# Optimization experiments

Hardware: AMD Instinct MI355X
Metric: run time of the kernel (lower is better)

The kernel has to match this reference:

```python
import jax, jax.numpy as jnp
import numpy as np

N_NODES = 100000
N_EDGES = 6400000


def setup_inputs() -> dict:
    key = jax.random.key(0)
    ks = jax.random.split(key, 20)
    g = lambda i, shape, fan_in: jax.random.normal(ks[i], shape, dtype=jnp.float32) / np.sqrt(fan_in)
    inp = {
        "x": jax.random.normal(ks[0], (N_NODES, 32), dtype=jnp.float32),
        "edge_index": jax.random.randint(ks[1], (2, N_EDGES), 0, N_NODES, dtype=jnp.int64),
        # encoder: Linear(32,240) -> ReLU -> Linear(240,24) -> ReLU
        "enc_w1": g(2, (32, 240), 32), "enc_b1": jnp.zeros((240,), jnp.float32),
        "enc_w2": g(3, (240, 24), 240), "enc_b2": jnp.zeros((24,), jnp.float32),
        # lin_r (applied to root, no bias) -- PyG defaults
        "sage1_wl": g(4, (24, 24), 24), "sage1_bl": jnp.zeros((24,), jnp.float32), "sage1_wr": g(5, (24, 24), 24),
        "sage2_wl": g(6, (24, 24), 24), "sage2_bl": jnp.zeros((24,), jnp.float32), "sage2_wr": g(7, (24, 24), 24),
        "sage3_wl": g(8, (24, 24), 24), "sage3_bl": jnp.zeros((24,), jnp.float32), "sage3_wr": g(9, (24, 24), 24),
        # decoder: Linear(24,120) -> ReLU -> Linear(120,12)
        "dec_w1": g(10, (24, 120), 24), "dec_b1": jnp.zeros((120,), jnp.float32),
        "dec_w2": g(11, (120, 12), 120), "dec_b2": jnp.zeros((12,), jnp.float32),
    }
    return inp


def _sage_conv(x, src, dst, wl, bl, wr, n_nodes):
    # mean aggregation: gather source features, scatter-sum at targets, divide by degree
    msg = x[src]                                                   # [E, H]
    agg = jax.ops.segment_sum(msg, dst, num_segments=n_nodes)      # [N, H]
    deg = jax.ops.segment_sum(jnp.ones((src.shape[0],), x.dtype), dst, num_segments=n_nodes)
    mean = agg / jnp.maximum(deg, 1.0)[:, None]
    return mean @ wl + bl + x @ wr


def reference(x, edge_index, enc_w1, enc_b1, enc_w2, enc_b2,
              sage1_wl, sage1_bl, sage1_wr,
              sage2_wl, sage2_bl, sage2_wr,
              sage3_wl, sage3_bl, sage3_wr,
              dec_w1, dec_b1, dec_w2, dec_b2):
    n = x.shape[0]
    src, dst = edge_index[0], edge_index[1]
    # encoder
    h = jax.nn.relu(x @ enc_w1 + enc_b1)
    h = jax.nn.relu(h @ enc_w2 + enc_b2)
    # GNN: SAGEConv -> ReLU -> SAGEConv -> ReLU -> SAGEConv
    h = jax.nn.relu(_sage_conv(h, src, dst, sage1_wl, sage1_bl, sage1_wr, n))
    h = jax.nn.relu(_sage_conv(h, src, dst, sage2_wl, sage2_bl, sage2_wr, n))
    h = _sage_conv(h, src, dst, sage3_wl, sage3_bl, sage3_wr, n)
    # decoder
    h = jax.nn.relu(h @ dec_w1 + dec_b1)
    return h @ dec_w2 + dec_b2
```

## Files before the change

kernel.cpp:

```cpp
#include <hip/hip_runtime.h>
#include <hip/hip_bf16.h>

#define N_NODES 100000
#define N_EDGES 6400000
#define BROW 24
#define PROW 8
#define BUCKET_SIZE 256
#define N_BUCKETS ((N_NODES + BUCKET_SIZE - 1) / BUCKET_SIZE)
#define BUCKET_CAP 17408
#define STAGE_CAP 22528
#define SENT 0xFFFFFFFFu
#define STAGE_BLOCKS 512
#define CHUNK ((N_EDGES + STAGE_BLOCKS - 1) / STAGE_BLOCKS)

typedef float floatx2 __attribute__((ext_vector_type(2)));

__device__ __forceinline__ unsigned short f2bf(float f) {
    unsigned u = __float_as_uint(f);
    unsigned r = (u + 0x7fffu + ((u >> 16) & 1u)) >> 16;
    return (unsigned short)r;
}

__device__ __forceinline__ unsigned pack_fp8_4(float a, float b, float c, float d) {
    int w = __builtin_amdgcn_cvt_pk_fp8_f32(a, b, 0, false);
    w = __builtin_amdgcn_cvt_pk_fp8_f32(c, d, w, true);
    return (unsigned)w;
}

#define DEC4(w, arr, j) { \
    floatx2 lo_ = __builtin_amdgcn_cvt_pk_f32_fp8((int)(w), false); \
    floatx2 hi_ = __builtin_amdgcn_cvt_pk_f32_fp8((int)(w), true);  \
    arr[j] += lo_.x; arr[(j)+1] += lo_.y; arr[(j)+2] += hi_.x; arr[(j)+3] += hi_.y; }

#define SET2(u, arr, j) { arr[j] = __uint_as_float((u) << 16); arr[(j)+1] = __uint_as_float((u) & 0xffff0000u); }
#define ADD2(u, arr, j) { arr[j] += __uint_as_float((u) << 16); arr[(j)+1] += __uint_as_float((u) & 0xffff0000u); }

__global__ __launch_bounds__(256) void k_transpose_w1(
    const float* __restrict__ w1, float* __restrict__ w1t)
{
    int tid = blockIdx.x * blockDim.x + threadIdx.x;
    if (tid < 32 * 240) {
        int k = tid >> 5, i = tid & 31;
        w1t[tid] = w1[i * 240 + k];
    }
}

__global__ __launch_bounds__(256) void k_stage1(
    const int* __restrict__ src, const int* __restrict__ dst,
    int* __restrict__ cursor, unsigned* __restrict__ stage)
{
    __shared__ int cnt[N_BUCKETS];
    __shared__ int bse[N_BUCKETS];
    __shared__ int lof[N_BUCKETS];
    __shared__ int cur[N_BUCKETS];
    __shared__ int ps[512];
    __shared__ unsigned sbuf[CHUNK];
    int t = threadIdx.x;
    int e0 = blockIdx.x * CHUNK;
    int e1 = min(e0 + CHUNK, N_EDGES);

    for (int i = t; i < N_BUCKETS; i += 256) cnt[i] = 0;
    __syncthreads();
    for (int e = e0 + t; e < e1; e += 256)
        atomicAdd(&cnt[dst[e] >> 8], 1);
    __syncthreads();
    for (int i = t; i < N_BUCKETS; i += 256) {
        int c = cnt[i];
        int c16 = (c + 15) & ~15;
        bse[i] = c16 ? atomicAdd(&cursor[i * 16], c16) : 0;
        cur[i] = 0;
    }
    ps[t]       = (t < N_BUCKETS) ? cnt[t] : 0;
    ps[t + 256] = (t + 256 < N_BUCKETS) ? cnt[t + 256] : 0;
    __syncthreads();
    for (int off = 1; off < 512; off <<= 1) {
        int a  = (t >= off) ? ps[t - off] : 0;
        int b2 = (t + 256 >= off) ? ps[t + 256 - off] : 0;
        __syncthreads();
        ps[t] += a;
        ps[t + 256] += b2;
        __syncthreads();
    }
    for (int i = t; i < N_BUCKETS; i += 256) lof[i] = ps[i] - cnt[i];
    __syncthreads();
    for (int e = e0 + t; e < e1; e += 256) {
        int d = dst[e];
        int s = src[e];
        int b = d >> 8;
        int pos = atomicAdd(&cur[b], 1);
        sbuf[lof[b] + pos] = ((unsigned)(d & 255) << 17) | (unsigned)s;
    }
    __syncthreads();
    int wid = t >> 6, lane = t & 63;
    for (int b = wid; b < N_BUCKETS; b += 4) {
        int c = cnt[b];
        int c16 = (c + 15) & ~15;
        unsigned* gp = stage + (size_t)b * STAGE_CAP + bse[b];
        const unsigned* lp = sbuf + lof[b];
        for (int j = lane; j < c16; j += 64)
            gp[j] = (j < c) ? lp[j] : SENT;
    }
}

__global__ __launch_bounds__(256) void k_fill_enc(
    const unsigned* __restrict__ stage, const int* __restrict__ cursor,
    int* __restrict__ csr, int* __restrict__ deg,
    float* __restrict__ recip, int* __restrict__ row_ptr,
    const float* __restrict__ x,
    const float* __restrict__ w1t, const float* __restrict__ b1,
    const float* __restrict__ w2,
    unsigned short* __restrict__ pb0, unsigned short* __restrict__ pb1)
{
    __shared__ int dl[BUCKET_SIZE];
    __shared__ int s[BUCKET_SIZE];
    __shared__ int fcur[BUCKET_SIZE];
    int t = threadIdx.x;

    if (blockIdx.x < N_BUCKETS) {
        int b = blockIdx.x;
        int ne = cursor[b * 16];
        const unsigned* sp = stage + (size_t)b * STAGE_CAP;

        dl[t] = 0;
        __syncthreads();
        for (int i = t; i < ne; i += 256) {
            unsigned v = sp[i];
            if (v != SENT) atomicAdd(&dl[v >> 17], 1);
        }
        __syncthreads();
        int d = dl[t];
        s[t] = d;
        __syncthreads();
        for (int off = 1; off < 256; off <<= 1) {
            int v = (t >= off) ? s[t - off] : 0;
            __syncthreads();
            s[t] += v;
            __syncthreads();
        }
        int excl = s[t] - d;
        fcur[t] = excl;
        int n = b * BUCKET_SIZE + t;
        if (n < N_NODES) {
            deg[n] = d;
            recip[n] = 1.0f / (float)max(d, 1);
            row_ptr[n] = b * BUCKET_CAP + excl;
        }
        __syncthreads();
        int* cb = csr + (size_t)b * BUCKET_CAP;
        for (int i = t; i < ne; i += 256) {
            unsigned v = sp[i];
            if (v == SENT) continue;
            int slot = atomicAdd(&fcur[v >> 17], 1);
            cb[slot] = (int)(v & 0x1FFFFu);
        }
    } else {
        int bid = blockIdx.x - N_BUCKETS;
        int nb = bid >> 1;
        int chunk = bid & 1;
        int n = nb * 256 + t;
        if (n >= N_NODES) return;

        float xr[32];
        const float4* xv = (const float4*)(x + (size_t)n * 32);
#pragma unroll
        for (int i = 0; i < 8; ++i) {
            float4 v = xv[i];
            xr[4*i+0] = v.x; xr[4*i+1] = v.y; xr[4*i+2] = v.z; xr[4*i+3] = v.w;
        }
        float acc[24];
#pragma unroll
        for (int j = 0; j < 24; ++j) acc[j] = 0.f;

        int k0 = chunk * 120;
        for (int k = k0; k < k0 + 120; ++k) {
            const float4* wr = (const float4*)(w1t + k * 32);
            float tt = b1[k];
#pragma unroll
            for (int q = 0; q < 8; ++q) {
                float4 w = wr[q];
                tt += xr[4*q+0] * w.x + xr[4*q+1] * w.y + xr[4*q+2] * w.z + xr[4*q+3] * w.w;
            }
            tt = fmaxf(tt, 0.f);
            const float* w2r = w2 + k * 24;
#pragma unroll
            for (int j = 0; j < 24; ++j) acc[j] += tt * w2r[j];
        }
        unsigned wb[12];
#pragma unroll
        for (int j = 0; j < 24; ++j) {
            if (j & 1) wb[j >> 1] |= (unsigned)f2bf(acc[j]) << 16;
            else       wb[j >> 1]  = (unsigned)f2bf(acc[j]);
        }
        unsigned short* pb = chunk ? pb1 : pb0;
        uint4* ob = (uint4*)(pb + (size_t)n * BROW);
#pragma unroll
        for (int q = 0; q < 3; ++q)
            ob[q] = make_uint4(wb[4*q], wb[4*q+1], wb[4*q+2], wb[4*q+3]);
    }
}

__global__ __launch_bounds__(256) void k_encfin_xform(
    const unsigned short* __restrict__ pb0, const unsigned short* __restrict__ pb1,
    const float* __restrict__ b2,
    const float* __restrict__ wl, const float* __restrict__ wr,
    unsigned* __restrict__ Ptab, float* __restrict__ Qtab)
{
    int n = blockIdx.x * blockDim.x + threadIdx.x;
    if (n >= N_NODES) return;
    float h[24];
    {
        const uint4* hp = (const uint4*)(pb0 + (size_t)n * BROW);
        uint4 A = hp[0], B = hp[1], C = hp[2];
        SET2(A.x, h, 0)  SET2(A.y, h, 2)  SET2(A.z, h, 4)  SET2(A.w, h, 6)
        SET2(B.x, h, 8)  SET2(B.y, h,10)  SET2(B.z, h,12)  SET2(B.w, h,14)
        SET2(C.x, h,16)  SET2(C.y, h,18)  SET2(C.z, h,20)  SET2(C.w, h,22)
    }
    {
        const uint4* hp = (const uint4*)(pb1 + (size_t)n * BROW);
        uint4 A = hp[0], B = hp[1], C = hp[2];
        ADD2(A.x, h, 0)  ADD2(A.y, h, 2)  ADD2(A.z, h, 4)  ADD2(A.w, h, 6)
        ADD2(B.x, h, 8)  ADD2(B.y, h,10)  ADD2(B.z, h,12)  ADD2(B.w, h,14)
        ADD2(C.x, h,16)  ADD2(C.y, h,18)  ADD2(C.z, h,20)  ADD2(C.w, h,22)
    }
#pragma unroll
    for (int j = 0; j < 24; ++j) h[j] = fmaxf(h[j] + b2[j], 0.f);

    float p[24], q[24];
#pragma unroll
    for (int j = 0; j < 24; ++j) { p[j] = 0.f; q[j] = 0.f; }
#pragma unroll
    for (int k = 0; k < 24; ++k) {
        float hk = h[k];
#pragma unroll
        for (int j = 0; j < 24; ++j) {
            p[j] += hk * wl[k * 24 + j];
            q[j] += hk * wr[k * 24 + j];
        }
    }
    unsigned w8[6];
#pragma unroll
    for (int c = 0; c < 6; ++c)
        w8[c] = pack_fp8_4(p[4*c], p[4*c+1], p[4*c+2], p[4*c+3]);
    uint4* ob = (uint4*)(Ptab + (size_t)n * PROW);
    ob[0] = make_uint4(w8[0], w8[1], w8[2], w8[3]);
    ob[1] = make_uint4(w8[4], w8[5], 0u, 0u);
    float4* qb = (float4*)(Qtab + n * 24);
#pragma unroll
    for (int c = 0; c < 6; ++c)
        qb[c] = make_float4(q[4*c], q[4*c+1], q[4*c+2], q[4*c+3]);
}

__global__ __launch_bounds__(256) void k_xform(
    const unsigned short* __restrict__ hin,
    const float* __restrict__ wl, const float* __restrict__ wr,
    unsigned* __restrict__ Ptab, float* __restrict__ Qtab)
{
    int n = blockIdx.x * blockDim.x + threadIdx.x;
    if (n >= N_NODES) return;
    float h[24];
    {
        const uint4* hp = (const uint4*)(hin + (size_t)n * BROW);
        uint4 A = hp[0], B = hp[1], C = hp[2];
        SET2(A.x, h, 0)  SET2(A.y, h, 2)  SET2(A.z, h, 4)  SET2(A.w, h, 6)
        SET2(B.x, h, 8)  SET2(B.y, h,10)  SET2(B.z, h,12)  SET2(B.w, h,14)
        SET2(C.x, h,16)  SET2(C.y, h,18)  SET2(C.z, h,20)  SET2(C.w, h,22)
    }
    float p[24], q[24];
#pragma unroll
    for (int j = 0; j < 24; ++j) { p[j] = 0.f; q[j] = 0.f; }
#pragma unroll
    for (int k = 0; k < 24; ++k) {
        float hk = h[k];
#pragma unroll
        for (int j = 0; j < 24; ++j) {
            p[j] += hk * wl[k * 24 + j];
            q[j] += hk * wr[k * 24 + j];
        }
    }
    unsigned w8[6];
#pragma unroll
    for (int c = 0; c < 6; ++c)
        w8[c] = pack_fp8_4(p[4*c], p[4*c+1], p[4*c+2], p[4*c+3]);
    uint4* ob = (uint4*)(Ptab + (size_t)n * PROW);
    ob[0] = make_uint4(w8[0], w8[1], w8[2], w8[3]);
    ob[1] = make_uint4(w8[4], w8[5], 0u, 0u);
    float4* qb = (float4*)(Qtab + n * 24);
#pragma unroll
    for (int c = 0; c < 6; ++c)
        qb[c] = make_float4(q[4*c], q[4*c+1], q[4*c+2], q[4*c+3]);
}

template <bool RELU>
__global__ __launch_bounds__(256, 4) void k_agg(
    const unsigned* __restrict__ Ptab, const float* __restrict__ Qtab,
    const int* __restrict__ row_ptr, const int* __restrict__ deg,
    const float* __restrict__ recip, const int* __restrict__ csr,
    const float* __restrict__ bl,
    unsigned short* __restrict__ houtb)
{
    int gt = blockIdx.x * blockDim.x + threadIdx.x;
    int n = gt >> 3, g = gt & 7;
    if (n >= N_NODES) return;
    int start = row_ptr[n];
    int cnt = deg[n];

    float acc[24];
#pragma unroll
    for (int j = 0; j < 24; ++j) acc[j] = 0.f;

    for (int i = g; i < cnt; i += 8) {
        int s = __builtin_nontemporal_load(&csr[start + i]);
        const uint4* rp = (const uint4*)(Ptab + (size_t)s * PROW);
        uint4 A = rp[0];
        uint2 B = ((const uint2*)rp)[2];
        DEC4(A.x, acc, 0)  DEC4(A.y, acc, 4)  DEC4(A.z, acc, 8)
        DEC4(A.w, acc,12)  DEC4(B.x, acc,16)  DEC4(B.y, acc,20)
    }
#pragma unroll
    for (int m = 1; m <= 4; m <<= 1)
#pragma unroll
        for (int j = 0; j < 24; ++j) acc[j] += __shfl_xor(acc[j], m, 64);

    if (g < 3) {
        float rc = recip[n];
        const float4* qb = (const float4*)(Qtab + n * 24 + g * 8);
        float4 q0 = qb[0], q1 = qb[1];
        float qv[8] = {q0.x, q0.y, q0.z, q0.w, q1.x, q1.y, q1.z, q1.w};
        unsigned wb[4];
#pragma unroll
        for (int jj = 0; jj < 8; ++jj) {
            int j = g * 8 + jj;
            float v = acc[j] * rc + qv[jj] + bl[j];
            if (RELU) v = fmaxf(v, 0.f);
            if (jj & 1) wb[jj >> 1] |= (unsigned)f2bf(v) << 16;
            else        wb[jj >> 1]  = (unsigned)f2bf(v);
        }
        ((uint4*)(houtb + (size_t)n * BROW))[g] = make_uint4(wb[0], wb[1], wb[2], wb[3]);
    }
}

__global__ __launch_bounds__(256, 4) void k_agg3(
    const unsigned* __restrict__ Ptab, const float* __restrict__ Qtab,
    const int* __restrict__ row_ptr, const int* __restrict__ deg,
    const float* __restrict__ recip, const int* __restrict__ csr,
    const float* __restrict__ bl,
    float* __restrict__ o3)
{
    int gt = blockIdx.x * blockDim.x + threadIdx.x;
    int n = gt >> 3, g = gt & 7;
    if (n >= N_NODES) return;
    int start = row_ptr[n];
    int cnt = deg[n];

    float acc[24];
#pragma unroll
    for (int j = 0; j < 24; ++j) acc[j] = 0.f;

    for (int i = g; i < cnt; i += 8) {
        int s = __builtin_nontemporal_load(&csr[start + i]);
        const uint4* rp = (const uint4*)(Ptab + (size_t)s * PROW);
        uint4 A = rp[0];
        uint2 B = ((const uint2*)rp)[2];
        DEC4(A.x, acc, 0)  DEC4(A.y, acc, 4)  DEC4(A.z, acc, 8)
        DEC4(A.w, acc,12)  DEC4(B.x, acc,16)  DEC4(B.y, acc,20)
    }
#pragma unroll
    for (int m = 1; m <= 4; m <<= 1)
#pragma unroll
        for (int j = 0; j < 24; ++j) acc[j] += __shfl_xor(acc[j], m, 64);

    if (g < 3) {
        float rc = recip[n];
        const float4* qb = (const float4*)(Qtab + n * 24 + g * 8);
        float4 q0 = qb[0], q1 = qb[1];
        float qv[8] = {q0.x, q0.y, q0.z, q0.w, q1.x, q1.y, q1.z, q1.w};
        float ov[8];
#pragma unroll
        for (int jj = 0; jj < 8; ++jj)
            ov[jj] = acc[g * 8 + jj] * rc + qv[jj] + bl[g * 8 + jj];
        float4* op = (float4*)(o3 + n * 24 + g * 8);
        op[0] = make_float4(ov[0], ov[1], ov[2], ov[3]);
        op[1] = make_float4(ov[4], ov[5], ov[6], ov[7]);
    }
}

__global__ __launch_bounds__(256) void k_decoder(
    const float* __restrict__ o3,
    const float* __restrict__ w1, const float* __restrict__ b1,
    const float* __restrict__ w2, const float* __restrict__ b2,
    float* __restrict__ out)
{
    int n = blockIdx.x * blockDim.x + threadIdx.x;
    if (n >= N_NODES) return;
    float h[24];
    const float4* hv = (const float4*)(o3 + (size_t)n * 24);
#pragma unroll
    for (int q = 0; q < 6; ++q) {
        float4 v = hv[q];
        h[4*q+0] = v.x; h[4*q+1] = v.y; h[4*q+2] = v.z; h[4*q+3] = v.w;
    }
    float acc[12];
#pragma unroll
    for (int j = 0; j < 12; ++j) acc[j] = b2[j];
    for (int k = 0; k < 120; ++k) {
        float t = b1[k];
#pragma unroll
        for (int i = 0; i < 24; ++i) t += h[i] * w1[i * 120 + k];
        t = fmaxf(t, 0.f);
#pragma unroll
        for (int j = 0; j < 12; ++j) acc[j] += t * w2[k * 12 + j];
    }
    float* o = out + (size_t)n * 12;
#pragma unroll
    for (int j = 0; j < 12; ++j) o[j] = acc[j];
}

static inline size_t align_up(size_t v, size_t a) { return (v + a - 1) & ~(a - 1); }

extern "C" void kernel_launch(void* const* d_in, const int* in_sizes, int n_in,
                              void* d_out, int out_size, void* d_ws, size_t ws_size,
                              hipStream_t stream)
{
    (void)in_sizes; (void)n_in; (void)out_size; (void)ws_size;

    const float* x    = (const float*)d_in[0];
    const int*  edge  = (const int*)d_in[1];
    const int*  esrc  = edge;
    const int*  edst  = edge + N_EDGES;
    const float* enc_w1 = (const float*)d_in[2];
    const float* enc_b1 = (const float*)d_in[3];
    const float* enc_w2 = (const float*)d_in[4];
    const float* enc_b2 = (const float*)d_in[5];
    const float* s1_wl = (const float*)d_in[6];
    const float* s1_bl = (const float*)d_in[7];
    const float* s1_wr = (const float*)d_in[8];
    const float* s2_wl = (const float*)d_in[9];
    const float* s2_bl = (const float*)d_in[10];
    const float* s2_wr = (const float*)d_in[11];
    const float* s3_wl = (const float*)d_in[12];
    const float* s3_bl = (const float*)d_in[13];
    const float* s3_wr = (const float*)d_in[14];
    const float* dec_w1 = (const float*)d_in[15];
    const float* dec_b1 = (const float*)d_in[16];
    const float* dec_w2 = (const float*)d_in[17];
    const float* dec_b2 = (const float*)d_in[18];
    float* out = (float*)d_out;

    char* base = (char*)d_ws;
    size_t off = 0;
    auto carve = [&](size_t bytes) { size_t o = off; off = align_up(off + bytes, 256); return (void*)(base + o); };
    char* stage_region = (char*)carve((size_t)N_BUCKETS * STAGE_CAP * sizeof(unsigned));
    unsigned* stage      = (unsigned*)stage_region;
    unsigned* Ptab       = (unsigned*)stage_region;
    float* Qtab          = (float*)(stage_region + 3200000);
    float* o3            = (float*)(stage_region + 12800000);
    int*   csr     = (int*)  carve((size_t)N_BUCKETS * BUCKET_CAP * sizeof(int));
    unsigned short* h0b = (unsigned short*)carve((size_t)N_NODES * BROW * sizeof(unsigned short));
    unsigned short* h1b = (unsigned short*)carve((size_t)N_NODES * BROW * sizeof(unsigned short));
    int*   deg     = (int*)  carve((size_t)N_NODES * sizeof(int));
    float* recip   = (float*)carve((size_t)N_NODES * sizeof(float));
    int*   row_ptr = (int*)  carve((size_t)N_NODES * sizeof(int));
    int*   cursor  = (int*)  carve((size_t)N_BUCKETS * 16 * sizeof(int));
    float* w1t     = (float*)carve((size_t)240 * 32 * sizeof(float));

    const int NB_N = (N_NODES + 255) / 256;
    const int NB8  = (N_NODES * 8 + 255) / 256;

    hipMemsetAsync(cursor, 0, (size_t)N_BUCKETS * 16 * sizeof(int), stream);
    k_transpose_w1<<<30, 256, 0, stream>>>(enc_w1, w1t);
    k_stage1<<<STAGE_BLOCKS, 256, 0, stream>>>(esrc, edst, cursor, stage);

    k_fill_enc<<<NB_N + NB_N * 2, 256, 0, stream>>>(
        stage, cursor, csr, deg, recip, row_ptr,
        x, w1t, enc_b1, enc_w2, h0b, h1b);

    k_encfin_xform<<<NB_N, 256, 0, stream>>>(h0b, h1b, enc_b2, s1_wl, s1_wr, Ptab, Qtab);
    k_agg<true><<<NB8, 256, 0, stream>>>(Ptab, Qtab, row_ptr, deg, recip, csr, s1_bl, h1b);
    k_xform<<<NB_N, 256, 0, stream>>>(h1b, s2_wl, s2_wr, Ptab, Qtab);
    k_agg<true><<<NB8, 256, 0, stream>>>(Ptab, Qtab, row_ptr, deg, recip, csr, s2_bl, h0b);
    k_xform<<<NB_N, 256, 0, stream>>>(h0b, s3_wl, s3_wr, Ptab, Qtab);
    k_agg3<<<NB8, 256, 0, stream>>>(Ptab, Qtab, row_ptr, deg, recip, csr, s3_bl, o3);
    k_decoder<<<NB_N, 256, 0, stream>>>(o3, dec_w1, dec_b1, dec_w2, dec_b2, out);
}
```

Before: 484.5 us.

## Fuse encoder into staging pass, pad CSR rows to 4, vectorize index loads

The encoder MLP blocks are interleaved into the edge-staging kernel, and the encoder finish plus first SAGE transform move into the CSR fill kernel. This removes one launch and lets the compute-heavy encoder overlap the memory-bound bucketing. Each CSR row is padded to a multiple of four with a sentinel index that points at a zeroed extra Ptab row, so the aggregation loops can read four neighbour indices with one int4 load. Ptab and Qtab get their own buffers instead of aliasing the staging region, and the bucket capacities grow to hold the padding, at the cost of extra workspace and some wasted gathers on padded slots.

Result: slower. 507.4 us (+4.7%).

```diff
diff --git a/kernel.cpp b/kernel.cpp
--- a/kernel.cpp
+++ b/kernel.cpp
@@ -7,11 +7,12 @@
 #define PROW 8
 #define BUCKET_SIZE 256
 #define N_BUCKETS ((N_NODES + BUCKET_SIZE - 1) / BUCKET_SIZE)
-#define BUCKET_CAP 17408
-#define STAGE_CAP 22528
+#define BUCKET_CAP 17920
+#define STAGE_CAP 26624
 #define SENT 0xFFFFFFFFu
-#define STAGE_BLOCKS 512
-#define CHUNK ((N_EDGES + STAGE_BLOCKS - 1) / STAGE_BLOCKS)
+#define STAGE_BLOCKS 1024
+#define CHUNK (N_EDGES / STAGE_BLOCKS)
+#define TOTAL_A (STAGE_BLOCKS + 2 * N_BUCKETS)
 
 typedef float floatx2 __attribute__((ext_vector_type(2)));
 
@@ -35,6 +36,13 @@
 #define SET2(u, arr, j) { arr[j] = __uint_as_float((u) << 16); arr[(j)+1] = __uint_as_float((u) & 0xffff0000u); }
 #define ADD2(u, arr, j) { arr[j] += __uint_as_float((u) << 16); arr[(j)+1] += __uint_as_float((u) & 0xffff0000u); }
 
+#define GATHER1(sidx, acc) { \
+    const uint4* rp_ = (const uint4*)(Ptab + (size_t)(sidx) * PROW); \
+    uint4 A_ = rp_[0]; \
+    uint2 B_ = ((const uint2*)rp_)[2]; \
+    DEC4(A_.x, acc, 0)  DEC4(A_.y, acc, 4)  DEC4(A_.z, acc, 8) \
+    DEC4(A_.w, acc,12)  DEC4(B_.x, acc,16)  DEC4(B_.y, acc,20) }
+
 __global__ __launch_bounds__(256) void k_transpose_w1(
     const float* __restrict__ w1, float* __restrict__ w1t)
 {
@@ -45,9 +53,13 @@
     }
 }
 
-__global__ __launch_bounds__(256) void k_stage1(
+__global__ __launch_bounds__(256) void k_stage_enc(
     const int* __restrict__ src, const int* __restrict__ dst,
-    int* __restrict__ cursor, unsigned* __restrict__ stage)
+    int* __restrict__ cursor, unsigned* __restrict__ stage,
+    const float* __restrict__ x,
+    const float* __restrict__ w1t, const float* __restrict__ b1,
+    const float* __restrict__ w2,
+    unsigned short* __restrict__ pb0, unsigned short* __restrict__ pb1)
 {
     __shared__ int cnt[N_BUCKETS];
     __shared__ int bse[N_BUCKETS];
@@ -56,60 +68,110 @@
     __shared__ int ps[512];
     __shared__ unsigned sbuf[CHUNK];
     int t = threadIdx.x;
-    int e0 = blockIdx.x * CHUNK;
-    int e1 = min(e0 + CHUNK, N_EDGES);
-
-    for (int i = t; i < N_BUCKETS; i += 256) cnt[i] = 0;
-    __syncthreads();
-    for (int e = e0 + t; e < e1; e += 256)
-        atomicAdd(&cnt[dst[e] >> 8], 1);
-    __syncthreads();
-    for (int i = t; i < N_BUCKETS; i += 256) {
-        int c = cnt[i];
-        int c16 = (c + 15) & ~15;
-        bse[i] = c16 ? atomicAdd(&cursor[i * 16], c16) : 0;
-        cur[i] = 0;
-    }
-    ps[t]       = (t < N_BUCKETS) ? cnt[t] : 0;
-    ps[t + 256] = (t + 256 < N_BUCKETS) ? cnt[t + 256] : 0;
-    __syncthreads();
-    for (int off = 1; off < 512; off <<= 1) {
-        int a  = (t >= off) ? ps[t - off] : 0;
-        int b2 = (t + 256 >= off) ? ps[t + 256 - off] : 0;
-        __syncthreads();
-        ps[t] += a;
-        ps[t + 256] += b2;
-        __syncthreads();
-    }
-    for (int i = t; i < N_BUCKETS; i += 256) lof[i] = ps[i] - cnt[i];
-    __syncthreads();
-    for (int e = e0 + t; e < e1; e += 256) {
-        int d = dst[e];
-        int s = src[e];
-        int b = d >> 8;
-        int pos = atomicAdd(&cur[b], 1);
-        sbuf[lof[b] + pos] = ((unsigned)(d & 255) << 17) | (unsigned)s;
-    }
-    __syncthreads();
-    int wid = t >> 6, lane = t & 63;
-    for (int b = wid; b < N_BUCKETS; b += 4) {
-        int c = cnt[b];
-        int c16 = (c + 15) & ~15;
-        unsigned* gp = stage + (size_t)b * STAGE_CAP + bse[b];
-        const unsigned* lp = sbuf + lof[b];
-        for (int j = lane; j < c16; j += 64)
-            gp[j] = (j < c) ? lp[j] : SENT;
-    }
-}
-
-__global__ __launch_bounds__(256) void k_fill_enc(
+
+    long long ii = blockIdx.x;
+    int a0 = (int)((ii * STAGE_BLOCKS) / TOTAL_A);
+    int a1 = (int)(((ii + 1) * STAGE_BLOCKS) / TOTAL_A);
+
+    if (a1 > a0) {
+        int e0 = a0 * CHUNK;
+        int e1 = min(e0 + CHUNK, N_EDGES);
+
+        for (int i = t; i < N_BUCKETS; i += 256) cnt[i] = 0;
+        __syncthreads();
+        for (int e = e0 + t; e < e1; e += 256)
+            atomicAdd(&cnt[dst[e] >> 8], 1);
+        __syncthreads();
+        for (int i = t; i < N_BUCKETS; i += 256) {
+            int c = cnt[i];
+            int c16 = (c + 15) & ~15;
+            bse[i] = c16 ? atomicAdd(&cursor[i * 16], c16) : 0;
+            cur[i] = 0;
+        }
+        ps[t]       = (t < N_BUCKETS) ? cnt[t] : 0;
+        ps[t + 256] = (t + 256 < N_BUCKETS) ? cnt[t + 256] : 0;
+        __syncthreads();
+        for (int off = 1; off < 512; off <<= 1) {
+            int a  = (t >= off) ? ps[t - off] : 0;
+            int b2 = (t + 256 >= off) ? ps[t + 256 - off] : 0;
+            __syncthreads();
+            ps[t] += a;
+            ps[t + 256] += b2;
+            __syncthreads();
+        }
+        for (int i = t; i < N_BUCKETS; i += 256) lof[i] = ps[i] - cnt[i];
+        __syncthreads();
+        for (int e = e0 + t; e < e1; e += 256) {
+            int d = dst[e];
+            int s = src[e];
+            int b = d >> 8;
+            int pos = atomicAdd(&cur[b], 1);
+            sbuf[lof[b] + pos] = ((unsigned)(d & 255) << 17) | (unsigned)s;
+        }
+        __syncthreads();
+        int wid = t >> 6, lane = t & 63;
+        for (int b = wid; b < N_BUCKETS; b += 4) {
+            int c = cnt[b];
+            int c16 = (c + 15) & ~15;
+            unsigned* gp = stage + (size_t)b * STAGE_CAP + bse[b];
+            const unsigned* lp = sbuf + lof[b];
+            for (int j = lane; j < c16; j += 64)
+                gp[j] = (j < c) ? lp[j] : SENT;
+        }
+    } else {
+        int eb = (int)(ii - a0);
+        int nb = eb >> 1;
+        int chunk = eb & 1;
+        int n = nb * 256 + t;
+        if (n >= N_NODES) return;
+
+        float xr[32];
+        const float4* xv = (const float4*)(x + (size_t)n * 32);
+#pragma unroll
+        for (int i = 0; i < 8; ++i) {
+            float4 v = xv[i];
+            xr[4*i+0] = v.x; xr[4*i+1] = v.y; xr[4*i+2] = v.z; xr[4*i+3] = v.w;
+        }
+        float acc[24];
+#pragma unroll
+        for (int j = 0; j < 24; ++j) acc[j] = 0.f;
+
+        int k0 = chunk * 120;
+        for (int k = k0; k < k0 + 120; ++k) {
+            const float4* wr = (const float4*)(w1t + k * 32);
+            float tt = b1[k];
+#pragma unroll
+            for (int q = 0; q < 8; ++q) {
+                float4 w = wr[q];
+                tt += xr[4*q+0] * w.x + xr[4*q+1] * w.y + xr[4*q+2] * w.z + xr[4*q+3] * w.w;
+            }
+            tt = fmaxf(tt, 0.f);
+            const float* w2r = w2 + k * 24;
+#pragma unroll
+            for (int j = 0; j < 24; ++j) acc[j] += tt * w2r[j];
+        }
+        unsigned wb[12];
+#pragma unroll
+        for (int j = 0; j < 24; ++j) {
+            if (j & 1) wb[j >> 1] |= (unsigned)f2bf(acc[j]) << 16;
+            else       wb[j >> 1]  = (unsigned)f2bf(acc[j]);
+        }
+        unsigned short* pb = chunk ? pb1 : pb0;
+        uint4* ob = (uint4*)(pb + (size_t)n * BROW);
+#pragma unroll
+        for (int q = 0; q < 3; ++q)
+            ob[q] = make_uint4(wb[4*q], wb[4*q+1], wb[4*q+2], wb[4*q+3]);
+    }
+}
+
+__global__ __launch_bounds__(256) void k_fill_encxf(
     const unsigned* __restrict__ stage, const int* __restrict__ cursor,
     int* __restrict__ csr, int* __restrict__ deg,
     float* __restrict__ recip, int* __restrict__ row_ptr,
-    const float* __restrict__ x,
-    const float* __restrict__ w1t, const float* __restrict__ b1,
-    const float* __restrict__ w2,
-    unsigned short* __restrict__ pb0, unsigned short* __restrict__ pb1)
+    const unsigned short* __restrict__ pb0, const unsigned short* __restrict__ pb1,
+    const float* __restrict__ b2,
+    const float* __restrict__ wl, const float* __restrict__ wr,
+    unsigned* __restrict__ Ptab, float* __restrict__ Qtab)
 {
     __shared__ int dl[BUCKET_SIZE];
     __shared__ int s[BUCKET_SIZE];
@@ -129,7 +191,8 @@
         }
         __syncthreads();
         int d = dl[t];
-        s[t] = d;
+        int d4 = (d + 3) & ~3;
+        s[t] = d4;
         __syncthreads();
         for (int off = 1; off < 256; off <<= 1) {
             int v = (t >= off) ? s[t - off] : 0;
@@ -137,7 +200,7 @@
             s[t] += v;
             __syncthreads();
         }
-        int excl = s[t] - d;
+        int excl = s[t] - d4;
         fcur[t] = excl;
         int n = b * BUCKET_SIZE + t;
         if (n < N_NODES) {
@@ -153,101 +216,60 @@
             int slot = atomicAdd(&fcur[v >> 17], 1);
             cb[slot] = (int)(v & 0x1FFFFu);
         }
+        __syncthreads();
+        if (n < N_NODES) {
+            for (int j = d; j < d4; ++j) cb[excl + j] = N_NODES;
+        }
     } else {
-        int bid = blockIdx.x - N_BUCKETS;
-        int nb = bid >> 1;
-        int chunk = bid & 1;
-        int n = nb * 256 + t;
+        int n = (blockIdx.x - N_BUCKETS) * 256 + t;
         if (n >= N_NODES) return;
-
-        float xr[32];
-        const float4* xv = (const float4*)(x + (size_t)n * 32);
-#pragma unroll
-        for (int i = 0; i < 8; ++i) {
-            float4 v = xv[i];
-            xr[4*i+0] = v.x; xr[4*i+1] = v.y; xr[4*i+2] = v.z; xr[4*i+3] = v.w;
-        }
-        float acc[24];
-#pragma unroll
-        for (int j = 0; j < 24; ++j) acc[j] = 0.f;
-
-        int k0 = chunk * 120;
-        for (int k = k0; k < k0 + 120; ++k) {
-            const float4* wr = (const float4*)(w1t + k * 32);
-            float tt = b1[k];
-#pragma unroll
-            for (int q = 0; q < 8; ++q) {
-                float4 w = wr[q];
-                tt += xr[4*q+0] * w.x + xr[4*q+1] * w.y + xr[4*q+2] * w.z + xr[4*q+3] * w.w;
+        float h[24];
+        {
+            const uint4* hp = (const uint4*)(pb0 + (size_t)n * BROW);
+            uint4 A = hp[0], B = hp[1], C = hp[2];
+            SET2(A.x, h, 0)  SET2(A.y, h, 2)  SET2(A.z, h, 4)  SET2(A.w, h, 6)
+            SET2(B.x, h, 8)  SET2(B.y, h,10)  SET2(B.z, h,12)  SET2(B.w, h,14)
+            SET2(C.x, h,16)  SET2(C.y, h,18)  SET2(C.z, h,20)  SET2(C.w, h,22)
+        }
+        {
+            const uint4* hp = (const uint4*)(pb1 + (size_t)n * BROW);
+            uint4 A = hp[0], B = hp[1], C = hp[2];
+            ADD2(A.x, h, 0)  ADD2(A.y, h, 2)  ADD2(A.z, h, 4)  ADD2(A.w, h, 6)
+            ADD2(B.x, h, 8)  ADD2(B.y, h,10)  ADD2(B.z, h,12)  ADD2(B.w, h,14)
+            ADD2(C.x, h,16)  ADD2(C.y, h,18)  ADD2(C.z, h,20)  ADD2(C.w, h,22)
+        }
+#pragma unroll
+        for (int j = 0; j < 24; ++j) h[j] = fmaxf(h[j] + b2[j], 0.f);
+
+        float p[24], q[24];
+#pragma unroll
+        for (int j = 0; j < 24; ++j) { p[j] = 0.f; q[j] = 0.f; }
+#pragma unroll
+        for (int k = 0; k < 24; ++k) {
+            float hk = h[k];
+#pragma unroll
+            for (int j = 0; j < 24; ++j) {
+                p[j] += hk * wl[k * 24 + j];
+                q[j] += hk * wr[k * 24 + j];
             }
-            tt = fmaxf(tt, 0.f);
-            const float* w2r = w2 + k * 24;
-#pragma unroll
-            for (int j = 0; j < 24; ++j) acc[j] += tt * w2r[j];
-        }
-        unsigned wb[12];
-#pragma unroll
-        for (int j = 0; j < 24; ++j) {
-            if (j & 1) wb[j >> 1] |= (unsigned)f2bf(acc[j]) << 16;
-            else       wb[j >> 1]  = (unsigned)f2bf(acc[j]);
-        }
-        unsigned short* pb = chunk ? pb1 : pb0;
-        uint4* ob = (uint4*)(pb + (size_t)n * BROW);
-#pragma unroll
-        for (int q = 0; q < 3; ++q)
-            ob[q] = make_uint4(wb[4*q], wb[4*q+1], wb[4*q+2], wb[4*q+3]);
-    }
-}
-
-__global__ __launch_bounds__(256) void k_encfin_xform(
-    const unsigned short* __restrict__ pb0, const unsigned short* __restrict__ pb1,
-    const float* __restrict__ b2,
-    const float* __restrict__ wl, const float* __restrict__ wr,
-    unsigned* __restrict__ Ptab, float* __restrict__ Qtab)
-{
-    int n = blockIdx.x * blockDim.x + threadIdx.x;
-    if (n >= N_NODES) return;
-    float h[24];
-    {
-        const uint4* hp = (const uint4*)(pb0 + (size_t)n * BROW);
-        uint4 A = hp[0], B = hp[1], C = hp[2];
-        SET2(A.x, h, 0)  SET2(A.y, h, 2)  SET2(A.z, h, 4)  SET2(A.w, h, 6)
-        SET2(B.x, h, 8)  SET2(B.y, h,10)  SET2(B.z, h,12)  SET2(B.w, h,14)
-        SET2(C.x, h,16)  SET2(C.y, h,18)  SET2(C.z, h,20)  SET2(C.w, h,22)
-    }
-    {
-        const uint4* hp = (const uint4*)(pb1 + (size_t)n * BROW);
-        uint4 A = hp[0], B = hp[1], C = hp[2];
-        ADD2(A.x, h, 0)  ADD2(A.y, h, 2)  ADD2(A.z, h, 4)  ADD2(A.w, h, 6)
-        ADD2(B.x, h, 8)  ADD2(B.y, h,10)  ADD2(B.z, h,12)  ADD2(B.w, h,14)
-        ADD2(C.x, h,16)  ADD2(C.y, h,18)  ADD2(C.z, h,20)  ADD2(C.w, h,22)
-    }
-#pragma unroll
-    for (int j = 0; j < 24; ++j) h[j] = fmaxf(h[j] + b2[j], 0.f);
-
-    float p[24], q[24];
-#pragma unroll
-    for (int j = 0; j < 24; ++j) { p[j] = 0.f; q[j] = 0.f; }
-#pragma unroll
-    for (int k = 0; k < 24; ++k) {
-        float hk = h[k];
-#pragma unroll
-        for (int j = 0; j < 24; ++j) {
-            p[j] += hk * wl[k * 24 + j];
-            q[j] += hk * wr[k * 24 + j];
-        }
-    }
-    unsigned w8[6];
-#pragma unroll
-    for (int c = 0; c < 6; ++c)
-        w8[c] = pack_fp8_4(p[4*c], p[4*c+1], p[4*c+2], p[4*c+3]);
-    uint4* ob = (uint4*)(Ptab + (size_t)n * PROW);
-    ob[0] = make_uint4(w8[0], w8[1], w8[2], w8[3]);
-    ob[1] = make_uint4(w8[4], w8[5], 0u, 0u);
-    float4* qb = (float4*)(Qtab + n * 24);
-#pragma unroll
-    for (int c = 0; c < 6; ++c)
-        qb[c] = make_float4(q[4*c], q[4*c+1], q[4*c+2], q[4*c+3]);
+        }
+        unsigned w8[6];
+#pragma unroll
+        for (int c = 0; c < 6; ++c)
+            w8[c] = pack_fp8_4(p[4*c], p[4*c+1], p[4*c+2], p[4*c+3]);
+        uint4* ob = (uint4*)(Ptab + (size_t)n * PROW);
+        ob[0] = make_uint4(w8[0], w8[1], w8[2], w8[3]);
+        ob[1] = make_uint4(w8[4], w8[5], 0u, 0u);
+        float4* qb = (float4*)(Qtab + (size_t)n * 24);
+#pragma unroll
+        for (int c = 0; c < 6; ++c)
+            qb[c] = make_float4(q[4*c], q[4*c+1], q[4*c+2], q[4*c+3]);
+        if (n == 0) {
+            uint4* zb = (uint4*)(Ptab + (size_t)N_NODES * PROW);
+            zb[0] = make_uint4(0u,0u,0u,0u);
+            zb[1] = make_uint4(0u,0u,0u,0u);
+        }
+    }
 }
 
 __global__ __launch_bounds__(256) void k_xform(
@@ -284,10 +306,15 @@
     uint4* ob = (uint4*)(Ptab + (size_t)n * PROW);
     ob[0] = make_uint4(w8[0], w8[1], w8[2], w8[3]);
     ob[1] = make_uint4(w8[4], w8[5], 0u, 0u);
-    float4* qb = (float4*)(Qtab + n * 24);
+    float4* qb = (float4*)(Qtab + (size_t)n * 24);
 #pragma unroll
     for (int c = 0; c < 6; ++c)
         qb[c] = make_float4(q[4*c], q[4*c+1], q[4*c+2], q[4*c+3]);
+    if (n == 0) {
+        uint4* zb = (uint4*)(Ptab + (size_t)N_NODES * PROW);
+        zb[0] = make_uint4(0u,0u,0u,0u);
+        zb[1] = make_uint4(0u,0u,0u,0u);
+    }
 }
 
 template <bool RELU>
@@ -302,19 +329,18 @@
     int n = gt >> 3, g = gt & 7;
     if (n >= N_NODES) return;
     int start = row_ptr[n];
-    int cnt = deg[n];
+    int cnt4 = (deg[n] + 3) & ~3;
 
     float acc[24];
 #pragma unroll
     for (int j = 0; j < 24; ++j) acc[j] = 0.f;
 
-    for (int i = g; i < cnt; i += 8) {
-        int s = __builtin_nontemporal_load(&csr[start + i]);
-        const uint4* rp = (const uint4*)(Ptab + (size_t)s * PROW);
-        uint4 A = rp[0];
-        uint2 B = ((const uint2*)rp)[2];
-        DEC4(A.x, acc, 0)  DEC4(A.y, acc, 4)  DEC4(A.z, acc, 8)
-        DEC4(A.w, acc,12)  DEC4(B.x, acc,16)  DEC4(B.y, acc,20)
+    for (int i0 = 4 * g; i0 < cnt4; i0 += 32) {
+        int4 s4 = *(const int4*)(csr + start + i0);
+        GATHER1(s4.x, acc)
+        GATHER1(s4.y, acc)
+        GATHER1(s4.z, acc)
+        GATHER1(s4.w, acc)
     }
 #pragma unroll
     for (int m = 1; m <= 4; m <<= 1)
@@ -323,7 +349,7 @@
 
     if (g < 3) {
         float rc = recip[n];
-        const float4* qb = (const float4*)(Qtab + n * 24 + g * 8);
+        const float4* qb = (const float4*)(Qtab + (size_t)n * 24 + g * 8);
         float4 q0 = qb[0], q1 = qb[1];
         float qv[8] = {q0.x, q0.y, q0.z, q0.w, q1.x, q1.y, q1.z, q1.w};
         unsigned wb[4];
@@ -350,19 +376,18 @@
     int n = gt >> 3, g = gt & 7;
     if (n >= N_NODES) return;
     int start = row_ptr[n];
-    int cnt = deg[n];
+    int cnt4 = (deg[n] + 3) & ~3;
 
     float acc[24];
 #pragma unroll
     for (int j = 0; j < 24; ++j) acc[j] = 0.f;
 
-    for (int i = g; i < cnt; i += 8) {
-        int s = __builtin_nontemporal_load(&csr[start + i]);
-        const uint4* rp = (const uint4*)(Ptab + (size_t)s * PROW);
-        uint4 A = rp[0];
-        uint2 B = ((const uint2*)rp)[2];
-        DEC4(A.x, acc, 0)  DEC4(A.y, acc, 4)  DEC4(A.z, acc, 8)
-        DEC4(A.w, acc,12)  DEC4(B.x, acc,16)  DEC4(B.y, acc,20)
+    for (int i0 = 4 * g; i0 < cnt4; i0 += 32) {
+        int4 s4 = *(const int4*)(csr + start + i0);
+        GATHER1(s4.x, acc)
+        GATHER1(s4.y, acc)
+        GATHER1(s4.z, acc)
+        GATHER1(s4.w, acc)
     }
 #pragma unroll
     for (int m = 1; m <= 4; m <<= 1)
@@ -371,14 +396,14 @@
 
     if (g < 3) {
         float rc = recip[n];
-        const float4* qb = (const float4*)(Qtab + n * 24 + g * 8);
+        const float4* qb = (const float4*)(Qtab + (size_t)n * 24 + g * 8);
         float4 q0 = qb[0], q1 = qb[1];
         float qv[8] = {q0.x, q0.y, q0.z, q0.w, q1.x, q1.y, q1.z, q1.w};
         float ov[8];
 #pragma unroll
         for (int jj = 0; jj < 8; ++jj)
             ov[jj] = acc[g * 8 + jj] * rc + qv[jj] + bl[g * 8 + jj];
-        float4* op = (float4*)(o3 + n * 24 + g * 8);
+        float4* op = (float4*)(o3 + (size_t)n * 24 + g * 8);
         op[0] = make_float4(ov[0], ov[1], ov[2], ov[3]);
         op[1] = make_float4(ov[4], ov[5], ov[6], ov[7]);
     }
@@ -450,11 +475,11 @@
     size_t off = 0;
     auto carve = [&](size_t bytes) { size_t o = off; off = align_up(off + bytes, 256); return (void*)(base + o); };
     char* stage_region = (char*)carve((size_t)N_BUCKETS * STAGE_CAP * sizeof(unsigned));
-    unsigned* stage      = (unsigned*)stage_region;
-    unsigned* Ptab       = (unsigned*)stage_region;
-    float* Qtab          = (float*)(stage_region + 3200000);
-    float* o3            = (float*)(stage_region + 12800000);
-    int*   csr     = (int*)  carve((size_t)N_BUCKETS * BUCKET_CAP * sizeof(int));
+    unsigned* stage = (unsigned*)stage_region;
+    float* o3       = (float*)stage_region;
+    int*   csr      = (int*)carve((size_t)N_BUCKETS * BUCKET_CAP * sizeof(int));
+    unsigned* Ptab  = (unsigned*)carve((size_t)(N_NODES + 1) * PROW * sizeof(unsigned));
+    float* Qtab     = (float*)carve((size_t)N_NODES * 24 * sizeof(float));
     unsigned short* h0b = (unsigned short*)carve((size_t)N_NODES * BROW * sizeof(unsigned short));
     unsigned short* h1b = (unsigned short*)carve((size_t)N_NODES * BROW * sizeof(unsigned short));
     int*   deg     = (int*)  carve((size_t)N_NODES * sizeof(int));
@@ -468,13 +493,14 @@
 
     hipMemsetAsync(cursor, 0, (size_t)N_BUCKETS * 16 * sizeof(int), stream);
     k_transpose_w1<<<30, 256, 0, stream>>>(enc_w1, w1t);
-    k_stage1<<<STAGE_BLOCKS, 256, 0, stream>>>(esrc, edst, cursor, stage);
-
-    k_fill_enc<<<NB_N + NB_N * 2, 256, 0, stream>>>(
+
+    k_stage_enc<<<TOTAL_A, 256, 0, stream>>>(
+        esrc, edst, cursor, stage, x, w1t, enc_b1, enc_w2, h0b, h1b);
+
+    k_fill_encxf<<<NB_N * 2, 256, 0, stream>>>(
         stage, cursor, csr, deg, recip, row_ptr,
-        x, w1t, enc_b1, enc_w2, h0b, h1b);
-
-    k_encfin_xform<<<NB_N, 256, 0, stream>>>(h0b, h1b, enc_b2, s1_wl, s1_wr, Ptab, Qtab);
+        h0b, h1b, enc_b2, s1_wl, s1_wr, Ptab, Qtab);
+
     k_agg<true><<<NB8, 256, 0, stream>>>(Ptab, Qtab, row_ptr, deg, recip, csr, s1_bl, h1b);
     k_xform<<<NB_N, 256, 0, stream>>>(h1b, s2_wl, s2_wr, Ptab, Qtab);
     k_agg<true><<<NB8, 256, 0, stream>>>(Ptab, Qtab, row_ptr, deg, recip, csr, s2_bl, h0b);
```
